# Optimization experiments

Measured on AMD Instinct MI355X. Metric: run time of the kernel, lower is better.

The kernel has to match this reference:

```python
import jax, jax.numpy as jnp
import numpy as np

BETA = 0.25
K = 1024   # num_codebook_vectors
D = 256    # latent_dim


def setup_inputs() -> dict:
    key = jax.random.key(0)
    k1, k2 = jax.random.split(key)
    z = jax.random.normal(k1, (32, D, 32, 32), dtype=jnp.float32)
    # original init: uniform(-1/K, 1/K)
    codebook = jax.random.uniform(k2, (K, D), dtype=jnp.float32, minval=-1.0 / K, maxval=1.0 / K)
    return {"z": z, "codebook": codebook}


def reference(z, codebook):
    B, C, H, W = z.shape
    sg = jax.lax.stop_gradient
    # NCHW -> NHWC, flatten to [N, D]
    z_nhwc = jnp.transpose(z, (0, 2, 3, 1))
    zf = z_nhwc.reshape(-1, C)
    # squared distances via sum-of-squares + matmul: [N, K]
    d = (jnp.sum(zf * zf, axis=1, keepdims=True)
         + jnp.sum(codebook * codebook, axis=1)
         - 2.0 * jnp.matmul(zf, codebook.T))
    idx = jnp.argmin(d, axis=1)                      # [N]
    z_q = codebook[idx].reshape(B, H, W, C)          # gather + reshape
    # commitment + codebook loss
    loss = (jnp.mean((sg(z_q) - z_nhwc) ** 2)
            + BETA * jnp.mean((z_q - sg(z_nhwc)) ** 2))
    # straight-through estimator
    z_q = z_nhwc + sg(z_q - z_nhwc)
    z_q = jnp.transpose(z_q, (0, 3, 1, 2))           # back to NCHW
    return z_q, idx, loss
```

## Files before the change

kernel.cpp:

```cpp
#include <hip/hip_runtime.h>

constexpr int D_ = 256;
constexpr int K_ = 1024;
constexpr int P_ = 1024;
constexpr int N_ = 32768;

constexpr int IDX_OFF  = 8388608;
constexpr int LOSS_OFF = 8421376;

constexpr int CB16_OFF = 0;
constexpr int CN_OFF   = 262400;
constexpr int ZN_OFF   = 263424;
constexpr int CNT_OFF  = 296448;
constexpr int WL_OFF   = 296449;

constexpr float RESCUE_MARGIN = 1e-4f;

typedef _Float16 half8 __attribute__((ext_vector_type(8)));
typedef float f32x4 __attribute__((ext_vector_type(4)));

__global__ __launch_bounds__(64) void vq_prep(const float* __restrict__ z,
                                              const float* __restrict__ cb,
                                              float* __restrict__ scratch,
                                              float* __restrict__ loss) {
  const int blk = blockIdx.x;
  const int lane = threadIdx.x;
  if (blk < 512) {
    const int n0 = blk * 64;
    const int b = n0 >> 10, p0 = n0 & (P_ - 1);
    const float* zp = z + (size_t)b * (D_ * P_) + p0 + lane;
    float a8[8];
    #pragma unroll
    for (int i = 0; i < 8; ++i) a8[i] = 0.0f;
    for (int oct = 0; oct < 32; ++oct) {
      #pragma unroll
      for (int i = 0; i < 8; ++i) {
        float v = zp[(size_t)(oct * 8 + i) * P_];
        a8[i] = fmaf(v, v, a8[i]);
      }
    }
    scratch[ZN_OFF + n0 + lane] = ((a8[0] + a8[1]) + (a8[2] + a8[3])) +
                                  ((a8[4] + a8[5]) + (a8[6] + a8[7]));
    if (blk == 0 && lane == 0) {
      *loss = 0.0f;
      ((int*)(scratch + CNT_OFF))[0] = 0;
    }
  } else if (blk < 1536) {
    const int k = blk - 512;
    const float* row = cb + (size_t)k * D_;
    double s = 0.0;
    #pragma unroll
    for (int i = 0; i < 4; ++i) {
      double v = (double)row[lane + i * 64];
      s = fma(v, v, s);
    }
    #pragma unroll
    for (int off = 32; off; off >>= 1) s += __shfl_down(s, off, 64);
    if (lane == 0) scratch[CN_OFF + k] = (float)s;
  } else {
    const int kt = blk - 1536;
    const int k = kt * 16 + (lane & 15);
    const int quad = lane >> 4;
    _Float16* cw = (_Float16*)(scratch + CB16_OFF);
    for (int ds = 0; ds < 8; ++ds) {
      const float* src = cb + (size_t)k * D_ + ds * 32 + quad * 8;
      half8 h, lo;
      #pragma unroll
      for (int j = 0; j < 8; ++j) {
        const float v = src[j] * 1024.0f;
        const _Float16 hh = (_Float16)v;
        h[j] = hh;
        lo[j] = (_Float16)(v - (float)hh);
      }
      const int s = kt * 8 + ds;
      *(half8*)(cw + ((size_t)(s * 2 + 0) * 64 + lane) * 8) = h;
      *(half8*)(cw + ((size_t)(s * 2 + 1) * 64 + lane) * 8) = lo;
    }
  }
}

__global__ __launch_bounds__(256, 2) void vq_mfma(const float* __restrict__ z,
                                                  float* __restrict__ scratch,
                                                  float* __restrict__ idxf) {
  const int t = threadIdx.x;
  const int w = t >> 6;
  const int l = t & 63;
  const int quad = l >> 4;
  const int col = l & 15;
  const int half = w >> 1;
  const int rpair = w & 1;
  const int n0 = blockIdx.x * 64;
  const int b = n0 >> 10;
  const int p0 = n0 & (P_ - 1);

  const _Float16* cbsw = (const _Float16*)(scratch + CB16_OFF);
  const float* cnorm = scratch + CN_OFF;
  const float* zn = scratch + ZN_OFF;

  __shared__ float Azs[64 * 33];
  __shared__ float sV1[2][64][16];
  __shared__ float sV2[2][64][16];
  __shared__ int   sI1[2][64][16];

  half8 Ah[2][8], Al[2][8];
  const int pp = t & 63;
  const int dl0 = (t >> 6) * 8;
  for (int ds = 0; ds < 8; ++ds) {
    __syncthreads();
    #pragma unroll
    for (int i = 0; i < 8; ++i) {
      const int dloc = dl0 + i;
      Azs[pp * 33 + dloc] =
          z[(size_t)b * (D_ * P_) + (size_t)(ds * 32 + dloc) * P_ + p0 + pp];
    }
    __syncthreads();
    #pragma unroll
    for (int rt = 0; rt < 2; ++rt) {
      const int row_local = (rpair * 2 + rt) * 16 + col;
      const float* src = &Azs[row_local * 33 + quad * 8];
      half8 h, lo;
      #pragma unroll
      for (int j = 0; j < 8; ++j) {
        const float v = src[j];
        const _Float16 hh = (_Float16)v;
        h[j] = hh;
        lo[j] = (_Float16)(v - (float)hh);
      }
      Ah[rt][ds] = h;
      Al[rt][ds] = lo;
    }
  }

  float znr[2][4];
  #pragma unroll
  for (int rt = 0; rt < 2; ++rt)
    #pragma unroll
    for (int r = 0; r < 4; ++r)
      znr[rt][r] = zn[n0 + (rpair * 2 + rt) * 16 + quad * 4 + r];

  float m1[2][4], m2v[2][4];
  int i1[2][4];
  #pragma unroll
  for (int rt = 0; rt < 2; ++rt)
    #pragma unroll
    for (int r = 0; r < 4; ++r) { m1[rt][r] = 1e30f; m2v[rt][r] = 1e30f; i1[rt][r] = 0; }

  const int kt0 = half * 32;
  half8 Bh[4], Bl[4];
  #pragma unroll
  for (int s = 0; s < 2; ++s) {
    const int sg = kt0 * 8 + s;
    Bh[s] = *(const half8*)(cbsw + ((size_t)(sg * 2 + 0) * 64 + l) * 8);
    Bl[s] = *(const half8*)(cbsw + ((size_t)(sg * 2 + 1) * 64 + l) * 8);
  }

  for (int kt = kt0; kt < kt0 + 32; ++kt) {
    f32x4 a0 = {0.f, 0.f, 0.f, 0.f};
    f32x4 a1 = {0.f, 0.f, 0.f, 0.f};
    const float cnf = cnorm[kt * 16 + col];
    #pragma unroll
    for (int ds = 0; ds < 8; ++ds) {
      const int s = kt * 8 + ds;
      const int cur = ds & 3;
      const int nx = (ds + 2) & 3;
      Bh[nx] = *(const half8*)(cbsw + ((size_t)((s + 2) * 2 + 0) * 64 + l) * 8);
      Bl[nx] = *(const half8*)(cbsw + ((size_t)((s + 2) * 2 + 1) * 64 + l) * 8);
      a0 = __builtin_amdgcn_mfma_f32_16x16x32_f16(Ah[0][ds], Bh[cur], a0, 0, 0, 0);
      a1 = __builtin_amdgcn_mfma_f32_16x16x32_f16(Ah[1][ds], Bh[cur], a1, 0, 0, 0);
      a0 = __builtin_amdgcn_mfma_f32_16x16x32_f16(Ah[0][ds], Bl[cur], a0, 0, 0, 0);
      a1 = __builtin_amdgcn_mfma_f32_16x16x32_f16(Ah[1][ds], Bl[cur], a1, 0, 0, 0);
      a0 = __builtin_amdgcn_mfma_f32_16x16x32_f16(Al[0][ds], Bh[cur], a0, 0, 0, 0);
      a1 = __builtin_amdgcn_mfma_f32_16x16x32_f16(Al[1][ds], Bh[cur], a1, 0, 0, 0);
    }
    const int kg = kt * 16 + col;
    #pragma unroll
    for (int r = 0; r < 4; ++r) {
      const float s0 = fmaf(a0[r], -0x1p-9f, znr[0][r] + cnf);
      if (s0 < m1[0][r]) { m2v[0][r] = m1[0][r]; m1[0][r] = s0; i1[0][r] = kg; }
      else if (s0 < m2v[0][r]) m2v[0][r] = s0;
      const float s1 = fmaf(a1[r], -0x1p-9f, znr[1][r] + cnf);
      if (s1 < m1[1][r]) { m2v[1][r] = m1[1][r]; m1[1][r] = s1; i1[1][r] = kg; }
      else if (s1 < m2v[1][r]) m2v[1][r] = s1;
    }
  }

  #pragma unroll
  for (int rt = 0; rt < 2; ++rt)
    #pragma unroll
    for (int r = 0; r < 4; ++r) {
      const int row_local = (rpair * 2 + rt) * 16 + quad * 4 + r;
      sV1[half][row_local][col] = m1[rt][r];
      sV2[half][row_local][col] = m2v[rt][r];
      sI1[half][row_local][col] = i1[rt][r];
    }
  __syncthreads();

  if (t < 64) {
    float V1 = 1e30f, V2 = 1e30f;
    int I1 = 0x7fffffff;
    for (int h = 0; h < 2; ++h)
      for (int c = 0; c < 16; ++c) {
        const float v1 = sV1[h][t][c], v2 = sV2[h][t][c];
        const int iv = sI1[h][t][c];
        if (v1 < V1)       { V2 = fminf(V1, v2); V1 = v1; I1 = iv; }
        else if (v1 == V1) { I1 = min(I1, iv); V2 = V1; }
        else               { V2 = fminf(V2, v1); }
      }
    idxf[n0 + t] = (float)I1;
    if (V2 - V1 < RESCUE_MARGIN) {
      int* cnt = (int*)(scratch + CNT_OFF);
      int* wl = (int*)(scratch + WL_OFF);
      const int pos = atomicAdd(cnt, 1);
      wl[pos] = n0 + t;
    }
  }
}

__global__ __launch_bounds__(256, 4) void vq_rescue(const float* __restrict__ z,
                                                    const float* __restrict__ cb,
                                                    const float* __restrict__ scratch,
                                                    float* __restrict__ idxf) {
  const int tid = threadIdx.x;
  const float* cnorm = scratch + CN_OFF;
  const float* zn = scratch + ZN_OFF;
  const int count = ((const int*)(scratch + CNT_OFF))[0];
  const int* wl = (const int*)(scratch + WL_OFF);

  __shared__ alignas(16) float zb[8][D_];
  __shared__ int nrow[8];
  __shared__ float rv[256];
  __shared__ int ri[256];

  for (int base = blockIdx.x * 8; base < count; base += gridDim.x * 8) {
    const int take = min(8, count - base);
    if (tid < 8) nrow[tid] = wl[base + (tid < take ? tid : 0)];
    __syncthreads();
    #pragma unroll
    for (int r = 0; r < 8; ++r) {
      const int n = nrow[r];
      const int b = n >> 10, p = n & (P_ - 1);
      zb[r][tid] = z[(size_t)b * (D_ * P_) + (size_t)tid * P_ + p];
    }
    __syncthreads();

    const int k0 = tid * 4;
    const float4* __restrict__ cr0 = (const float4*)(cb + (size_t)(k0 + 0) * D_);
    const float4* __restrict__ cr1 = (const float4*)(cb + (size_t)(k0 + 1) * D_);
    const float4* __restrict__ cr2 = (const float4*)(cb + (size_t)(k0 + 2) * D_);
    const float4* __restrict__ cr3 = (const float4*)(cb + (size_t)(k0 + 3) * D_);

    float acc[8][4];
    #pragma unroll
    for (int r = 0; r < 8; ++r)
      #pragma unroll
      for (int j = 0; j < 4; ++j) acc[r][j] = 0.0f;

    for (int d4 = 0; d4 < 64; ++d4) {
      const float4 v0 = cr0[d4], v1 = cr1[d4], v2 = cr2[d4], v3 = cr3[d4];
      #pragma unroll
      for (int r = 0; r < 8; ++r) {
        const float4 zv = ((const float4*)zb[r])[d4];
        acc[r][0] = fmaf(zv.x, v0.x, acc[r][0]);
        acc[r][0] = fmaf(zv.y, v0.y, acc[r][0]);
        acc[r][0] = fmaf(zv.z, v0.z, acc[r][0]);
        acc[r][0] = fmaf(zv.w, v0.w, acc[r][0]);
        acc[r][1] = fmaf(zv.x, v1.x, acc[r][1]);
        acc[r][1] = fmaf(zv.y, v1.y, acc[r][1]);
        acc[r][1] = fmaf(zv.z, v1.z, acc[r][1]);
        acc[r][1] = fmaf(zv.w, v1.w, acc[r][1]);
        acc[r][2] = fmaf(zv.x, v2.x, acc[r][2]);
        acc[r][2] = fmaf(zv.y, v2.y, acc[r][2]);
        acc[r][2] = fmaf(zv.z, v2.z, acc[r][2]);
        acc[r][2] = fmaf(zv.w, v2.w, acc[r][2]);
        acc[r][3] = fmaf(zv.x, v3.x, acc[r][3]);
        acc[r][3] = fmaf(zv.y, v3.y, acc[r][3]);
        acc[r][3] = fmaf(zv.z, v3.z, acc[r][3]);
        acc[r][3] = fmaf(zv.w, v3.w, acc[r][3]);
      }
    }

    for (int r = 0; r < 8; ++r) {
      const int n = nrow[r];
      const float zA = zn[n];
      float bv = 1e30f;
      int bi = 0x7fffffff;
      #pragma unroll
      for (int j = 0; j < 4; ++j) {
        const float A = zA + cnorm[k0 + j];
        const float s = A - 2.0f * acc[r][j];
        if (s < bv) { bv = s; bi = k0 + j; }
      }
      rv[tid] = bv; ri[tid] = bi;
      __syncthreads();
      for (int off = 128; off >= 1; off >>= 1) {
        if (tid < off) {
          const float ov = rv[tid + off];
          const int oi = ri[tid + off];
          if (ov < rv[tid] || (ov == rv[tid] && oi < ri[tid])) { rv[tid] = ov; ri[tid] = oi; }
        }
        __syncthreads();
      }
      if (tid == 0 && r < take) idxf[n] = (float)ri[0];
      __syncthreads();
    }
  }
}

__global__ __launch_bounds__(256) void vq_gather(const float* __restrict__ z,
                                                 const float* __restrict__ cb,
                                                 const float* __restrict__ idxf,
                                                 float* __restrict__ out,
                                                 float* __restrict__ loss) {
  const int tid = threadIdx.x;
  const int lane = tid & 63;
  const int w = tid >> 6;
  const int n0 = blockIdx.x * 64;
  const int b = n0 >> 10;
  const int p0 = n0 & (P_ - 1);
  const int p = p0 + lane;

  const int idx = (int)(idxf[n0 + lane] + 0.5f);
  const float4* crow4 = (const float4*)(cb + (size_t)idx * D_);
  const size_t base = (size_t)b * (D_ * P_) + p;

  float acc = 0.0f;
  #pragma unroll 4
  for (int ci = 0; ci < 16; ++ci) {
    const float4 v = crow4[w * 16 + ci];
    const int c = w * 64 + ci * 4;
    const float vv[4] = {v.x, v.y, v.z, v.w};
    #pragma unroll
    for (int u = 0; u < 4; ++u) {
      const size_t a = base + (size_t)(c + u) * P_;
      const float zv = z[a];
      const float d = vv[u] - zv;
      out[a] = zv + d;
      acc = fmaf(d, d, acc);
    }
  }
  #pragma unroll
  for (int off = 32; off; off >>= 1) acc += __shfl_down(acc, off, 64);
  __shared__ float wsum[4];
  if (lane == 0) wsum[w] = acc;
  __syncthreads();
  if (tid == 0) {
    float s = wsum[0] + wsum[1] + wsum[2] + wsum[3];
    atomicAdd(loss, s * (1.25f / 8388608.0f));
  }
}

extern "C" void kernel_launch(void* const* d_in, const int* in_sizes, int n_in,
                              void* d_out, int out_size, void* d_ws, size_t ws_size,
                              hipStream_t stream) {
  const float* z = (const float*)d_in[0];
  const float* cb = (const float*)d_in[1];
  float* out = (float*)d_out;

  vq_prep<<<1600, 64, 0, stream>>>(z, cb, out, out + LOSS_OFF);
  vq_mfma<<<N_ / 64, 256, 0, stream>>>(z, out, out + IDX_OFF);
  vq_rescue<<<128, 256, 0, stream>>>(z, cb, out, out + IDX_OFF);
  vq_gather<<<N_ / 64, 256, 0, stream>>>(z, cb, out + IDX_OFF, out, out + LOSS_OFF);
}
```

Measured before the change: 255.2 us.

## Stage codebook through LDS with async triple-buffered loads and per-wave row tiles

Each wave now owns 16 rows across all 1024 codes. The split-fp16 codebook tiles are staged into a shared triple buffer with global_load_lds, so the four waves share one copy instead of each loading it from global memory into registers. The block-level LDS argmin merge is replaced by a wave-level shuffle reduction, and code norms are cached in LDS. It adds one barrier per code tile and manual vmcnt waits, and the K-dimension split into two accumulators cuts the MFMA parallelism per wave.

Measured after the change: 251.5 us. No clear change (-1.4%).

```diff
diff --git a/kernel.cpp b/kernel.cpp
--- a/kernel.cpp
+++ b/kernel.cpp
@@ -18,6 +18,12 @@
 
 typedef _Float16 half8 __attribute__((ext_vector_type(8)));
 typedef float f32x4 __attribute__((ext_vector_type(4)));
+
+__device__ __forceinline__ void stage16(const float* g, float* l) {
+  __builtin_amdgcn_global_load_lds(
+      (const __attribute__((address_space(1))) unsigned int*)g,
+      (__attribute__((address_space(3))) unsigned int*)l, 16, 0, 0);
+}
 
 __global__ __launch_bounds__(64) void vq_prep(const float* __restrict__ z,
                                               const float* __restrict__ cb,
@@ -87,24 +93,26 @@
   const int l = t & 63;
   const int quad = l >> 4;
   const int col = l & 15;
-  const int half = w >> 1;
-  const int rpair = w & 1;
   const int n0 = blockIdx.x * 64;
   const int b = n0 >> 10;
   const int p0 = n0 & (P_ - 1);
 
-  const _Float16* cbsw = (const _Float16*)(scratch + CB16_OFF);
-  const float* cnorm = scratch + CN_OFF;
-  const float* zn = scratch + ZN_OFF;
-
-  __shared__ float Azs[64 * 33];
-  __shared__ float sV1[2][64][16];
-  __shared__ float sV2[2][64][16];
-  __shared__ int   sI1[2][64][16];
-
-  half8 Ah[2][8], Al[2][8];
-  const int pp = t & 63;
-  const int dl0 = (t >> 6) * 8;
+  const float* __restrict__ cbsw_f = scratch + CB16_OFF;
+  const float* __restrict__ cnorm = scratch + CN_OFF;
+  const float* __restrict__ zn = scratch + ZN_OFF;
+
+  __shared__ alignas(16) float Bbuf[3][4096];
+  __shared__ alignas(16) float cnLds[1024];
+  float* Azs = &Bbuf[2][0];
+
+  *(float4*)(cnLds + t * 4) = *(const float4*)(cnorm + t * 4);
+
+  const float4 znv = *(const float4*)(zn + n0 + w * 16 + quad * 4);
+  float znr[4] = {znv.x, znv.y, znv.z, znv.w};
+
+  half8 Ah[8], Al[8];
+  const int pp = l;
+  const int dl0 = w * 8;
   for (int ds = 0; ds < 8; ++ds) {
     __syncthreads();
     #pragma unroll
@@ -114,9 +122,8 @@
           z[(size_t)b * (D_ * P_) + (size_t)(ds * 32 + dloc) * P_ + p0 + pp];
     }
     __syncthreads();
-    #pragma unroll
-    for (int rt = 0; rt < 2; ++rt) {
-      const int row_local = (rpair * 2 + rt) * 16 + col;
+    {
+      const int row_local = w * 16 + col;
       const float* src = &Azs[row_local * 33 + quad * 8];
       half8 h, lo;
       #pragma unroll
@@ -126,92 +133,112 @@
         h[j] = hh;
         lo[j] = (_Float16)(v - (float)hh);
       }
-      Ah[rt][ds] = h;
-      Al[rt][ds] = lo;
-    }
-  }
-
-  float znr[2][4];
+      Ah[ds] = h;
+      Al[ds] = lo;
+    }
+  }
+
+  {
+    const float* g0 = cbsw_f + l * 4;
+    #pragma unroll
+    for (int j = 0; j < 4; ++j) {
+      const int chunk = w * 4 + j;
+      stage16(g0 + chunk * 256, &Bbuf[0][chunk * 256]);
+    }
+    #pragma unroll
+    for (int j = 0; j < 4; ++j) {
+      const int chunk = w * 4 + j;
+      stage16(g0 + 4096 + chunk * 256, &Bbuf[1][chunk * 256]);
+    }
+  }
+
+  float m1[4], m2v[4];
+  int i1[4];
   #pragma unroll
-  for (int rt = 0; rt < 2; ++rt)
-    #pragma unroll
-    for (int r = 0; r < 4; ++r)
-      znr[rt][r] = zn[n0 + (rpair * 2 + rt) * 16 + quad * 4 + r];
-
-  float m1[2][4], m2v[2][4];
-  int i1[2][4];
-  #pragma unroll
-  for (int rt = 0; rt < 2; ++rt)
-    #pragma unroll
-    for (int r = 0; r < 4; ++r) { m1[rt][r] = 1e30f; m2v[rt][r] = 1e30f; i1[rt][r] = 0; }
-
-  const int kt0 = half * 32;
-  half8 Bh[4], Bl[4];
-  #pragma unroll
-  for (int s = 0; s < 2; ++s) {
-    const int sg = kt0 * 8 + s;
-    Bh[s] = *(const half8*)(cbsw + ((size_t)(sg * 2 + 0) * 64 + l) * 8);
-    Bl[s] = *(const half8*)(cbsw + ((size_t)(sg * 2 + 1) * 64 + l) * 8);
-  }
-
-  for (int kt = kt0; kt < kt0 + 32; ++kt) {
+  for (int r = 0; r < 4; ++r) { m1[r] = 1e30f; m2v[r] = 1e30f; i1[r] = 0; }
+
+  int cur = 0, stg = 2;
+  const float* gs = cbsw_f + 2 * 4096 + l * 4;
+
+  for (int kt = 0; kt < 64; ++kt) {
+    if (kt < 63) {
+      asm volatile("s_waitcnt vmcnt(4)" ::: "memory");
+    } else {
+      asm volatile("s_waitcnt vmcnt(0)" ::: "memory");
+    }
+    __builtin_amdgcn_s_barrier();
+    __builtin_amdgcn_sched_barrier(0);
+
+    if (kt < 62) {
+      float* db = &Bbuf[stg][0];
+      #pragma unroll
+      for (int j = 0; j < 4; ++j) {
+        const int chunk = w * 4 + j;
+        stage16(gs + chunk * 256, db + chunk * 256);
+      }
+      gs += 4096;
+    }
+
+    const float* bb = &Bbuf[cur][0];
+    const float cnf = cnLds[(kt << 4) + col];
     f32x4 a0 = {0.f, 0.f, 0.f, 0.f};
     f32x4 a1 = {0.f, 0.f, 0.f, 0.f};
-    const float cnf = cnorm[kt * 16 + col];
-    #pragma unroll
-    for (int ds = 0; ds < 8; ++ds) {
-      const int s = kt * 8 + ds;
-      const int cur = ds & 3;
-      const int nx = (ds + 2) & 3;
-      Bh[nx] = *(const half8*)(cbsw + ((size_t)((s + 2) * 2 + 0) * 64 + l) * 8);
-      Bl[nx] = *(const half8*)(cbsw + ((size_t)((s + 2) * 2 + 1) * 64 + l) * 8);
-      a0 = __builtin_amdgcn_mfma_f32_16x16x32_f16(Ah[0][ds], Bh[cur], a0, 0, 0, 0);
-      a1 = __builtin_amdgcn_mfma_f32_16x16x32_f16(Ah[1][ds], Bh[cur], a1, 0, 0, 0);
-      a0 = __builtin_amdgcn_mfma_f32_16x16x32_f16(Ah[0][ds], Bl[cur], a0, 0, 0, 0);
-      a1 = __builtin_amdgcn_mfma_f32_16x16x32_f16(Ah[1][ds], Bl[cur], a1, 0, 0, 0);
-      a0 = __builtin_amdgcn_mfma_f32_16x16x32_f16(Al[0][ds], Bh[cur], a0, 0, 0, 0);
-      a1 = __builtin_amdgcn_mfma_f32_16x16x32_f16(Al[1][ds], Bh[cur], a1, 0, 0, 0);
-    }
-    const int kg = kt * 16 + col;
+
+    __builtin_amdgcn_s_setprio(1);
+    #pragma unroll
+    for (int ds = 0; ds < 4; ++ds) {
+      const half8 bh = *(const half8*)(bb + (ds * 2 + 0) * 256 + l * 4);
+      const half8 bl = *(const half8*)(bb + (ds * 2 + 1) * 256 + l * 4);
+      a0 = __builtin_amdgcn_mfma_f32_16x16x32_f16(Ah[ds], bh, a0, 0, 0, 0);
+      a0 = __builtin_amdgcn_mfma_f32_16x16x32_f16(Ah[ds], bl, a0, 0, 0, 0);
+      a0 = __builtin_amdgcn_mfma_f32_16x16x32_f16(Al[ds], bh, a0, 0, 0, 0);
+    }
+    #pragma unroll
+    for (int ds = 4; ds < 8; ++ds) {
+      const half8 bh = *(const half8*)(bb + (ds * 2 + 0) * 256 + l * 4);
+      const half8 bl = *(const half8*)(bb + (ds * 2 + 1) * 256 + l * 4);
+      a1 = __builtin_amdgcn_mfma_f32_16x16x32_f16(Ah[ds], bh, a1, 0, 0, 0);
+      a1 = __builtin_amdgcn_mfma_f32_16x16x32_f16(Ah[ds], bl, a1, 0, 0, 0);
+      a1 = __builtin_amdgcn_mfma_f32_16x16x32_f16(Al[ds], bh, a1, 0, 0, 0);
+    }
+    __builtin_amdgcn_s_setprio(0);
+
+    const int kg = (kt << 4) + col;
     #pragma unroll
     for (int r = 0; r < 4; ++r) {
-      const float s0 = fmaf(a0[r], -0x1p-9f, znr[0][r] + cnf);
-      if (s0 < m1[0][r]) { m2v[0][r] = m1[0][r]; m1[0][r] = s0; i1[0][r] = kg; }
-      else if (s0 < m2v[0][r]) m2v[0][r] = s0;
-      const float s1 = fmaf(a1[r], -0x1p-9f, znr[1][r] + cnf);
-      if (s1 < m1[1][r]) { m2v[1][r] = m1[1][r]; m1[1][r] = s1; i1[1][r] = kg; }
-      else if (s1 < m2v[1][r]) m2v[1][r] = s1;
-    }
+      const float s0 = fmaf(a0[r] + a1[r], -0x1p-9f, znr[r] + cnf);
+      if (s0 < m1[r]) { m2v[r] = m1[r]; m1[r] = s0; i1[r] = kg; }
+      else if (s0 < m2v[r]) m2v[r] = s0;
+    }
+
+    cur = (cur == 2) ? 0 : cur + 1;
+    stg = (stg == 2) ? 0 : stg + 1;
   }
 
   #pragma unroll
-  for (int rt = 0; rt < 2; ++rt)
+  for (int off = 1; off <= 8; off <<= 1) {
     #pragma unroll
     for (int r = 0; r < 4; ++r) {
-      const int row_local = (rpair * 2 + rt) * 16 + quad * 4 + r;
-      sV1[half][row_local][col] = m1[rt][r];
-      sV2[half][row_local][col] = m2v[rt][r];
-      sI1[half][row_local][col] = i1[rt][r];
-    }
-  __syncthreads();
-
-  if (t < 64) {
-    float V1 = 1e30f, V2 = 1e30f;
-    int I1 = 0x7fffffff;
-    for (int h = 0; h < 2; ++h)
-      for (int c = 0; c < 16; ++c) {
-        const float v1 = sV1[h][t][c], v2 = sV2[h][t][c];
-        const int iv = sI1[h][t][c];
-        if (v1 < V1)       { V2 = fminf(V1, v2); V1 = v1; I1 = iv; }
-        else if (v1 == V1) { I1 = min(I1, iv); V2 = V1; }
-        else               { V2 = fminf(V2, v1); }
-      }
-    idxf[n0 + t] = (float)I1;
-    if (V2 - V1 < RESCUE_MARGIN) {
-      int* cnt = (int*)(scratch + CNT_OFF);
-      int* wl = (int*)(scratch + WL_OFF);
-      const int pos = atomicAdd(cnt, 1);
-      wl[pos] = n0 + t;
+      const float o1 = __shfl_xor(m1[r], off, 64);
+      const float o2 = __shfl_xor(m2v[r], off, 64);
+      const int oi = __shfl_xor(i1[r], off, 64);
+      if (o1 < m1[r]) { m2v[r] = fminf(m1[r], o2); m1[r] = o1; i1[r] = oi; }
+      else if (o1 == m1[r]) { i1[r] = min(i1[r], oi); m2v[r] = m1[r]; }
+      else { m2v[r] = fminf(m2v[r], o1); }
+    }
+  }
+
+  if (col == 0) {
+    int* cnt = (int*)(scratch + CNT_OFF);
+    int* wl = (int*)(scratch + WL_OFF);
+    #pragma unroll
+    for (int r = 0; r < 4; ++r) {
+      const int n = n0 + w * 16 + quad * 4 + r;
+      idxf[n] = (float)i1[r];
+      if (m2v[r] - m1[r] < RESCUE_MARGIN) {
+        const int pos = atomicAdd(cnt, 1);
+        wl[pos] = n;
+      }
     }
   }
 }
```
